# Kernel tuning notes

Hardware: AMD Instinct MI355X
Metric: run time of the kernel (lower is better)

## Reference

```python
import jax, jax.numpy as jnp
import numpy as np

B, S, H = 2, 2048, 2048
NH, NKV, HD = 16, 4, 128
GROUPS = NH // NKV
THETA = 10000.0
EPS = 1e-6


def setup_inputs() -> dict:
    key = jax.random.key(0)
    ks = jax.random.split(key, 6)
    scale = 0.02
    return {
        "hidden_states": jax.random.normal(ks[0], (B, S, H), jnp.float32),
        "wq": jax.random.normal(ks[1], (NH * HD, H), jnp.float32) * scale,
        "wk": jax.random.normal(ks[2], (NKV * HD, H), jnp.float32) * scale,
        "wv": jax.random.normal(ks[3], (NKV * HD, H), jnp.float32) * scale,
        "wo": jax.random.normal(ks[4], (H, NH * HD), jnp.float32) * scale,
        "q_norm_weight": jnp.ones((HD,), jnp.float32),
        "k_norm_weight": jnp.ones((HD,), jnp.float32),
    }


def _rope_tables(seq_len):
    inv_freq = 1.0 / (THETA ** (jnp.arange(0, HD, 2, dtype=jnp.float32) / HD))
    t = jnp.arange(seq_len, dtype=jnp.float32)
    freqs = jnp.outer(t, inv_freq)              # [S, HD/2]
    emb = jnp.concatenate([freqs, freqs], -1)   # [S, HD]
    return jnp.cos(emb), jnp.sin(emb)


def _rotate_half(x):
    x1, x2 = x[..., : HD // 2], x[..., HD // 2:]
    return jnp.concatenate([-x2, x1], -1)


def _rmsnorm(x, w):
    var = jnp.mean(jnp.square(x), axis=-1, keepdims=True)
    return x * jax.lax.rsqrt(var + EPS) * w


def reference(hidden_states, wq, wk, wv, wo, q_norm_weight, k_norm_weight):
    b, s, _ = hidden_states.shape
    q = (hidden_states @ wq.T).reshape(b, s, NH, HD).transpose(0, 2, 1, 3)    # [b,nh,s,d]
    k = (hidden_states @ wk.T).reshape(b, s, NKV, HD).transpose(0, 2, 1, 3)   # [b,nkv,s,d]
    v = (hidden_states @ wv.T).reshape(b, s, NKV, HD).transpose(0, 2, 1, 3)

    cos, sin = _rope_tables(s)                  # [s,d]
    q = q * cos + _rotate_half(q) * sin
    k = k * cos + _rotate_half(k) * sin

    # fused QK RMSNorm (applied inside fused_qknorm_flash_attention)
    q = _rmsnorm(q, q_norm_weight)
    k = _rmsnorm(k, k_norm_weight)

    # GQA: share each kv head across GROUPS query heads without materializing repeats
    qg = q.reshape(b, NKV, GROUPS, s, HD)
    scale = 1.0 / jnp.sqrt(jnp.float32(HD))
    scores = jnp.einsum('bhgqd,bhkd->bhgqk', qg, k) * scale   # [b,nkv,g,s,s]
    causal = jnp.tril(jnp.ones((s, s), bool))
    scores = jnp.where(causal, scores, jnp.finfo(scores.dtype).min)
    probs = jax.nn.softmax(scores, axis=-1)
    out = jnp.einsum('bhgqk,bhkd->bhgqd', probs, v)            # [b,nkv,g,s,d]
    out = out.reshape(b, NH, s, HD).transpose(0, 2, 1, 3).reshape(b, s, NH * HD)
    return out @ wo.T
```

## Files before the change

### kernel.cpp

```cpp
#include <hip/hip_runtime.h>
#include <math.h>

typedef __bf16 bf16;
typedef __bf16 bf16x8 __attribute__((ext_vector_type(8)));
typedef __bf16 bf16x4 __attribute__((ext_vector_type(4)));
typedef float f32x4 __attribute__((ext_vector_type(4)));

#define B_DIM 2
#define S_LEN 2048
#define H_DIM 2048
#define NH 16
#define NKV 4
#define HD 128

__device__ __forceinline__ void gl_lds16(const void* g, void* l) {
    __builtin_amdgcn_global_load_lds(
        (const __attribute__((address_space(1))) unsigned int*)g,
        (__attribute__((address_space(3))) unsigned int*)l, 16, 0, 0);
}

__global__ __launch_bounds__(256) void cast_all(const float* __restrict__ s0,
                                                const float* __restrict__ s1,
                                                const float* __restrict__ s2,
                                                const float* __restrict__ s3,
                                                const float* __restrict__ s4,
                                                bf16* __restrict__ dst) {
    const int i = blockIdx.x * 256 + threadIdx.x;
    const float* src;
    int off;
    if (i < 2097152)      { src = s0; off = 0; }
    else if (i < 3145728) { src = s1; off = 2097152; }
    else if (i < 3407872) { src = s2; off = 3145728; }
    else if (i < 3670016) { src = s3; off = 3407872; }
    else                  { src = s4; off = 3670016; }
    float4 f = ((const float4*)src)[i - off];
    bf16x4 o = { (bf16)f.x, (bf16)f.y, (bf16)f.z, (bf16)f.w };
    *(bf16x4*)(dst + (size_t)i * 4) = o;
}

template <typename OutT>
__global__ __launch_bounds__(256) void gemm_bt(const bf16* __restrict__ A,
                                               const bf16* __restrict__ Bt,
                                               OutT* __restrict__ C,
                                               int M, int N, int K) {
    __shared__ __align__(16) bf16 As[128 * 32];
    __shared__ __align__(16) bf16 Bs[128 * 32];
    const int t = threadIdx.x;
    const int lane = t & 63, w = t >> 6;
    const int wm = (w & 1) * 64, wn = (w >> 1) * 64;
    const int lr = lane & 15, quad = lane >> 4;
    const int m0 = blockIdx.x * 128, n0 = blockIdx.y * 128;
    const int lrow = lane >> 2, lk = (lane & 3) * 8;
    f32x4 acc[4][4];
#pragma unroll
    for (int i = 0; i < 4; i++)
#pragma unroll
        for (int j = 0; j < 4; j++) acc[i][j] = (f32x4){0.f, 0.f, 0.f, 0.f};

    for (int k0 = 0; k0 < K; k0 += 32) {
        __syncthreads();
#pragma unroll
        for (int i = 0; i < 2; i++) {
            const int r0 = i * 64 + w * 16;
            gl_lds16(A + (size_t)(m0 + r0 + lrow) * K + k0 + lk, &As[r0 * 32]);
            gl_lds16(Bt + (size_t)(n0 + r0 + lrow) * K + k0 + lk, &Bs[r0 * 32]);
        }
        __syncthreads();
        bf16x8 af[4], bfr[4];
#pragma unroll
        for (int i = 0; i < 4; i++) af[i] = *(const bf16x8*)&As[(wm + i * 16 + lr) * 32 + quad * 8];
#pragma unroll
        for (int j = 0; j < 4; j++) bfr[j] = *(const bf16x8*)&Bs[(wn + j * 16 + lr) * 32 + quad * 8];
#pragma unroll
        for (int i = 0; i < 4; i++)
#pragma unroll
            for (int j = 0; j < 4; j++)
                acc[i][j] = __builtin_amdgcn_mfma_f32_16x16x32_bf16(af[i], bfr[j], acc[i][j], 0, 0, 0);
    }
#pragma unroll
    for (int i = 0; i < 4; i++) {
        int m = m0 + wm + i * 16 + quad * 4;
#pragma unroll
        for (int j = 0; j < 4; j++) {
            int n = n0 + wn + j * 16 + lr;
#pragma unroll
            for (int r = 0; r < 4; r++)
                C[(size_t)(m + r) * N + n] = (OutT)acc[i][j][r];
        }
    }
}

__global__ __launch_bounds__(256) void rope_rms(const bf16* __restrict__ qkv,
                                                const float* __restrict__ qw,
                                                const float* __restrict__ kw,
                                                bf16* __restrict__ qb,
                                                bf16* __restrict__ kb,
                                                bf16* __restrict__ vt) {
    const int tok = blockIdx.x;
    const int b = tok >> 11, s = tok & (S_LEN - 1);
    const int lane = threadIdx.x & 63, w = threadIdx.x >> 6;
    const bf16* row = qkv + (size_t)tok * 3072;
    const float inv = expf(-(float)lane * (9.210340371976184f / 64.f));
    const float ang = (float)s * inv;
    float s_, c_;
    sincosf(ang, &s_, &c_);
    const float wq1 = qw[lane], wq2 = qw[lane + 64];
    const float wk1 = kw[lane], wk2 = kw[lane + 64];
    for (int u = w; u < 24; u += 4) {
        if (u < 16) {
            const float x1 = (float)row[u * 128 + lane], x2 = (float)row[u * 128 + 64 + lane];
            float y1 = x1 * c_ - x2 * s_;
            float y2 = x2 * c_ + x1 * s_;
            float ss = y1 * y1 + y2 * y2;
#pragma unroll
            for (int m = 1; m < 64; m <<= 1) ss += __shfl_xor(ss, m);
            const float r = rsqrtf(ss * (1.f / 128.f) + 1e-6f);
            size_t o = ((size_t)(b * NH + u) * S_LEN + s) * HD;
            qb[o + lane]      = (bf16)(y1 * r * wq1);
            qb[o + 64 + lane] = (bf16)(y2 * r * wq2);
        } else if (u < 20) {
            const int kh = u - 16;
            const float x1 = (float)row[2048 + kh * 128 + lane], x2 = (float)row[2048 + kh * 128 + 64 + lane];
            float y1 = x1 * c_ - x2 * s_;
            float y2 = x2 * c_ + x1 * s_;
            float ss = y1 * y1 + y2 * y2;
#pragma unroll
            for (int m = 1; m < 64; m <<= 1) ss += __shfl_xor(ss, m);
            const float r = rsqrtf(ss * (1.f / 128.f) + 1e-6f);
            size_t base = (size_t)(b * NKV + kh) * 16 * 16384;
            kb[base + (size_t)(lane >> 3) * 16384 + s * 8 + (lane & 7)]       = (bf16)(y1 * r * wk1);
            kb[base + (size_t)(8 + (lane >> 3)) * 16384 + s * 8 + (lane & 7)] = (bf16)(y2 * r * wk2);
        } else {
            const int vh = u - 20;
            const float x1 = (float)row[2560 + vh * 128 + lane], x2 = (float)row[2560 + vh * 128 + 64 + lane];
            const int m = s & 31;
            const int gi = (s >> 5) * 4 + ((m & 15) >> 2);
            const int el = ((m >> 4) << 2) | (m & 3);
            size_t base = ((size_t)(b * NKV + vh) * 256 + gi) * 1024 + el;
            vt[base + (size_t)lane * 8]        = (bf16)x1;
            vt[base + (size_t)(lane + 64) * 8] = (bf16)x2;
        }
    }
}

__global__ __launch_bounds__(256, 2) void flash(const bf16* __restrict__ qg,
                                                const bf16* __restrict__ kg,
                                                const bf16* __restrict__ vg,
                                                bf16* __restrict__ attn) {
    const int idx = blockIdx.x;
    const int g = idx >> 5;
    const int qt = (g < 8) ? (15 - g) : (g - 8);
    const int hb = idx & 31;
    const int h = hb & 15, b = hb >> 4;
    const int kvh = h >> 2;
    const bf16* qh = qg + (size_t)(b * NH + h) * S_LEN * HD;
    const bf16* kh = kg + (size_t)(b * NKV + kvh) * (16 * 16384);
    const bf16* vh = vg + (size_t)(b * NKV + kvh) * (256 * 1024);
    __shared__ __align__(16) bf16 Ks[2][16 * 512];
    __shared__ __align__(16) bf16 Vs[2][8 * 1024];
    const int t = threadIdx.x, lane = t & 63, w = t >> 6, lr = lane & 15, quad = lane >> 4;
    const int row0 = qt * 128 + w * 32;
    bf16x8 qf[2][4];
#pragma unroll
    for (int mg = 0; mg < 2; mg++)
#pragma unroll
        for (int c = 0; c < 4; c++)
            qf[mg][c] = *(const bf16x8*)(qh + (size_t)(row0 + mg * 16 + lr) * HD + c * 32 + quad * 8);
    f32x4 o[2][8];
    f32x4 lacc[2];
#pragma unroll
    for (int mg = 0; mg < 2; mg++) {
        lacc[mg] = (f32x4){0.f, 0.f, 0.f, 0.f};
#pragma unroll
        for (int j = 0; j < 8; j++) o[mg][j] = (f32x4){0.f, 0.f, 0.f, 0.f};
    }
    const bf16 one = (bf16)1.0f;
    const bf16x8 ones8 = {one, one, one, one, one, one, one, one};
    const float C1 = 0.12751744f;
    const float C2 = -17.3123405f;
    const int ntile = 2 * qt + 2;

    auto stage = [&](int kt_, int bi) {
        const int kb = kt_ * 64;
#pragma unroll
        for (int i = 0; i < 4; i++) {
            const int dc = w * 4 + i;
            gl_lds16(kh + (size_t)dc * 16384 + (size_t)kb * 8 + lane * 8, &Ks[bi][dc * 512]);
        }
#pragma unroll
        for (int i = 0; i < 2; i++) {
            const int c = w * 2 + i;
            const bf16* src = vh + (size_t)(8 * kt_ + ((c >> 2) << 2) + (c & 3)) * 1024 + lane * 8;
            gl_lds16(src, &Vs[bi][c * 1024]);
            gl_lds16(src + 512, &Vs[bi][c * 1024 + 512]);
        }
    };

    stage(0, 0);
    __syncthreads();
    int cur = 0;

    for (int kt = 0; kt < ntile; ++kt) {
        const int kbase = kt * 64;
        if (kt + 1 < ntile) stage(kt + 1, cur ^ 1);
        f32x4 sacc[2][4];
#pragma unroll
        for (int mg = 0; mg < 2; mg++)
#pragma unroll
            for (int n = 0; n < 4; n++) sacc[mg][n] = (f32x4){0.f, 0.f, 0.f, 0.f};
#pragma unroll
        for (int n = 0; n < 4; n++)
#pragma unroll
            for (int c = 0; c < 4; c++) {
                bf16x8 kf = *(const bf16x8*)&Ks[cur][(c * 4 + quad) * 512 + (n * 16 + lr) * 8];
                sacc[0][n] = __builtin_amdgcn_mfma_f32_16x16x32_bf16(kf, qf[0][c], sacc[0][n], 0, 0, 0);
                sacc[1][n] = __builtin_amdgcn_mfma_f32_16x16x32_bf16(kf, qf[1][c], sacc[1][n], 0, 0, 0);
            }
        const bool diag = (kt >= 2 * qt);
        bf16x8 pT[2][2];
#pragma unroll
        for (int mg = 0; mg < 2; mg++) {
            const int qrow = row0 + mg * 16 + lr;
#pragma unroll
            for (int n = 0; n < 4; n++)
#pragma unroll
                for (int r = 0; r < 4; r++) {
                    float ev = exp2f(fmaf(sacc[mg][n][r], C1, C2));
                    if (diag) {
                        const int key = kbase + n * 16 + quad * 4 + r;
                        ev = (key <= qrow) ? ev : 0.f;
                    }
                    pT[mg][n >> 1][(n & 1) * 4 + r] = (bf16)ev;
                }
        }
#pragma unroll
        for (int k2 = 0; k2 < 2; k2++) {
#pragma unroll
            for (int j = 0; j < 8; j++) {
                bf16x8 vf = *(const bf16x8*)&Vs[cur][(k2 * 4 + quad) * 1024 + (j * 16 + lr) * 8];
                o[0][j] = __builtin_amdgcn_mfma_f32_16x16x32_bf16(vf, pT[0][k2], o[0][j], 0, 0, 0);
                o[1][j] = __builtin_amdgcn_mfma_f32_16x16x32_bf16(vf, pT[1][k2], o[1][j], 0, 0, 0);
            }
            lacc[0] = __builtin_amdgcn_mfma_f32_16x16x32_bf16(ones8, pT[0][k2], lacc[0], 0, 0, 0);
            lacc[1] = __builtin_amdgcn_mfma_f32_16x16x32_bf16(ones8, pT[1][k2], lacc[1], 0, 0, 0);
        }
        __syncthreads();
        cur ^= 1;
    }
#pragma unroll
    for (int mg = 0; mg < 2; mg++) {
        const float inv = 1.0f / lacc[mg][0];
        const int qrow = row0 + mg * 16 + lr;
        bf16* dst = attn + ((size_t)(b * S_LEN) + qrow) * (NH * HD) + h * HD + quad * 4;
#pragma unroll
        for (int j = 0; j < 8; j++) {
            bf16x4 st = { (bf16)(o[mg][j][0] * inv), (bf16)(o[mg][j][1] * inv),
                          (bf16)(o[mg][j][2] * inv), (bf16)(o[mg][j][3] * inv) };
            *(bf16x4*)(dst + j * 16) = st;
        }
    }
}

extern "C" void kernel_launch(void* const* d_in, const int* in_sizes, int n_in,
                              void* d_out, int out_size, void* d_ws, size_t ws_size,
                              hipStream_t stream) {
    (void)in_sizes; (void)n_in; (void)out_size; (void)ws_size;
    const float* hs  = (const float*)d_in[0];
    const float* wq  = (const float*)d_in[1];
    const float* wk  = (const float*)d_in[2];
    const float* wv  = (const float*)d_in[3];
    const float* wo  = (const float*)d_in[4];
    const float* qnw = (const float*)d_in[5];
    const float* knw = (const float*)d_in[6];
    float* out = (float*)d_out;

    char* ws = (char*)d_ws;
    size_t off = 0;
    auto alloc = [&](size_t bytes) {
        void* p = ws + off;
        off += (bytes + 255) & ~(size_t)255;
        return p;
    };
    bf16* hs_bf   = (bf16*)alloc((size_t)4096 * 2048 * 2);
    bf16* wqkv_bf = (bf16*)alloc((size_t)3072 * 2048 * 2);
    bf16* wo_bf   = (bf16*)alloc((size_t)2048 * 2048 * 2);
    bf16* qkv_bf  = (bf16*)alloc((size_t)4096 * 3072 * 2);
    bf16* q_bf    = (bf16*)alloc((size_t)B_DIM * NH * S_LEN * HD * 2);
    bf16* k_bf    = (bf16*)alloc((size_t)B_DIM * NKV * S_LEN * HD * 2);
    bf16* vt_bf   = (bf16*)alloc((size_t)B_DIM * NKV * S_LEN * HD * 2);
    bf16* at_bf   = (bf16*)alloc((size_t)4096 * 2048 * 2);

    cast_all<<<18432, 256, 0, stream>>>(hs, wq, wk, wv, wo, hs_bf);
    gemm_bt<bf16><<<dim3(32, 24), 256, 0, stream>>>(hs_bf, wqkv_bf, qkv_bf, 4096, 3072, 2048);
    rope_rms<<<4096, 256, 0, stream>>>(qkv_bf, qnw, knw, q_bf, k_bf, vt_bf);
    flash<<<dim3(512), 256, 0, stream>>>(q_bf, k_bf, vt_bf, at_bf);
    gemm_bt<float><<<dim3(32, 16), 256, 0, stream>>>(at_bf, wo_bf, out, 4096, 2048, 2048);
}
```

Measured before the change: 325.3 us.

## Replace 128x128 GEMM with 256x256 double-buffered 8-wave pipelined GEMM

Replaces the simple 128x128-tile, single-buffered GEMM with a 256x256-tile kernel using 512 threads, 128 KB of LDS, and double-buffered global-to-LDS loads interleaved with MFMA phases. It also adds an XOR swizzle on LDS columns to avoid bank conflicts, a workgroup remapping across XCDs, and s_setprio around the MFMA bursts. The aim is more data reuse per tile and overlap of loads with compute. In exchange the grid is small (192 and 128 blocks), which may underfill the 256 CUs, and the hand-rolled waitcnt and barrier scheme is fragile.

```diff
diff --git a/kernel.cpp b/kernel.cpp
--- a/kernel.cpp
+++ b/kernel.cpp
@@ -17,6 +17,12 @@
     __builtin_amdgcn_global_load_lds(
         (const __attribute__((address_space(1))) unsigned int*)g,
         (__attribute__((address_space(3))) unsigned int*)l, 16, 0, 0);
+}
+
+__device__ __forceinline__ void bar() {
+    asm volatile("" ::: "memory");
+    __builtin_amdgcn_s_barrier();
+    asm volatile("" ::: "memory");
 }
 
 __global__ __launch_bounds__(256) void cast_all(const float* __restrict__ s0,
@@ -39,53 +45,135 @@
 }
 
 template <typename OutT>
-__global__ __launch_bounds__(256) void gemm_bt(const bf16* __restrict__ A,
-                                               const bf16* __restrict__ Bt,
-                                               OutT* __restrict__ C,
-                                               int M, int N, int K) {
-    __shared__ __align__(16) bf16 As[128 * 32];
-    __shared__ __align__(16) bf16 Bs[128 * 32];
-    const int t = threadIdx.x;
-    const int lane = t & 63, w = t >> 6;
-    const int wm = (w & 1) * 64, wn = (w >> 1) * 64;
+__global__ __launch_bounds__(512, 2) void gemm256(const bf16* __restrict__ A,
+                                                  const bf16* __restrict__ Bt,
+                                                  OutT* __restrict__ C,
+                                                  int M, int N, int K) {
+    __shared__ __align__(16) bf16 smem[65536];
+    const int t = threadIdx.x, lane = t & 63, w = t >> 6;
     const int lr = lane & 15, quad = lane >> 4;
-    const int m0 = blockIdx.x * 128, n0 = blockIdx.y * 128;
-    const int lrow = lane >> 2, lk = (lane & 3) * 8;
-    f32x4 acc[4][4];
-#pragma unroll
-    for (int i = 0; i < 4; i++)
+    const int nN = N >> 8;
+    const int nwg = gridDim.x, chunk = nwg >> 3;
+    const int bid = blockIdx.x;
+    const int lid = (bid & 7) * chunk + (bid >> 3);
+    const int m0 = (lid / nN) << 8, n0 = (lid % nN) << 8;
+    const int mh_w = w >> 2;
+    const int wn = (w & 3) << 6;
+    const int nh_w = (w & 3) >> 1;
+    const int rb = (w & 1) << 6;
+    const int nK = K >> 6;
+    const int nIter = K >> 7;
+
+    const int ld0 = w * 2;
+    const int lrow = lane >> 2;
+    const int csrc = (lane & 3) ^ ((lane >> 5) << 1);
+    const int swz = (lr >> 3) << 1;
+
+    auto stA = [&](int ts, int mh) {
+        if (ts < nK) {
+            bf16* db = smem + (ts & 1) * 16384 + mh * 8192;
+            const bf16* sp = A + (size_t)(m0 + mh * 128) * K + ts * 64;
+#pragma unroll
+            for (int i = 0; i < 2; i++) {
+                const int ldi = ld0 + i, kb = ldi >> 3, rg = ldi & 7;
+                gl_lds16(sp + (size_t)(rg * 16 + lrow) * K + kb * 32 + csrc * 8,
+                         db + kb * 4096 + rg * 512);
+            }
+        }
+    };
+    auto stB = [&](int ts, int nh) {
+        if (ts < nK) {
+            bf16* db = smem + 32768 + (ts & 1) * 16384 + nh * 8192;
+            const bf16* sp = Bt + (size_t)(n0 + nh * 128) * K + ts * 64;
+#pragma unroll
+            for (int i = 0; i < 2; i++) {
+                const int ldi = ld0 + i, kb = ldi >> 3, rg = ldi & 7;
+                gl_lds16(sp + (size_t)(rg * 16 + lrow) * K + kb * 32 + csrc * 8,
+                         db + kb * 4096 + rg * 512);
+            }
+        }
+    };
+
+    f32x4 acc[8][4];
+#pragma unroll
+    for (int i = 0; i < 8; i++)
 #pragma unroll
         for (int j = 0; j < 4; j++) acc[i][j] = (f32x4){0.f, 0.f, 0.f, 0.f};
-
-    for (int k0 = 0; k0 < K; k0 += 32) {
-        __syncthreads();
-#pragma unroll
-        for (int i = 0; i < 2; i++) {
-            const int r0 = i * 64 + w * 16;
-            gl_lds16(A + (size_t)(m0 + r0 + lrow) * K + k0 + lk, &As[r0 * 32]);
-            gl_lds16(Bt + (size_t)(n0 + r0 + lrow) * K + k0 + lk, &Bs[r0 * 32]);
-        }
-        __syncthreads();
-        bf16x8 af[4], bfr[4];
-#pragma unroll
-        for (int i = 0; i < 4; i++) af[i] = *(const bf16x8*)&As[(wm + i * 16 + lr) * 32 + quad * 8];
-#pragma unroll
-        for (int j = 0; j < 4; j++) bfr[j] = *(const bf16x8*)&Bs[(wn + j * 16 + lr) * 32 + quad * 8];
-#pragma unroll
-        for (int i = 0; i < 4; i++)
-#pragma unroll
-            for (int j = 0; j < 4; j++)
-                acc[i][j] = __builtin_amdgcn_mfma_f32_16x16x32_bf16(af[i], bfr[j], acc[i][j], 0, 0, 0);
-    }
-#pragma unroll
-    for (int i = 0; i < 4; i++) {
-        int m = m0 + wm + i * 16 + quad * 4;
-#pragma unroll
-        for (int j = 0; j < 4; j++) {
-            int n = n0 + wn + j * 16 + lr;
+    bf16x8 af[8], b0[4], b1[4];
+
+    auto rdA = [&](int s, int fi0) {
+        const bf16* bp = smem + s * 16384 + mh_w * 8192;
+#pragma unroll
+        for (int f = 0; f < 4; f++)
+#pragma unroll
+            for (int ks = 0; ks < 2; ks++)
+                af[f * 2 + ks] = *(const bf16x8*)(bp + ks * 4096 +
+                                                  ((fi0 + f) * 16 + lr) * 32 + (quad ^ swz) * 8);
+    };
+    auto rdB = [&](int s, int fj0, bf16x8* dst) {
+        const bf16* bp = smem + 32768 + s * 16384 + nh_w * 8192;
+#pragma unroll
+        for (int f = 0; f < 2; f++)
+#pragma unroll
+            for (int ks = 0; ks < 2; ks++)
+                dst[f * 2 + ks] = *(const bf16x8*)(bp + ks * 4096 +
+                                                   (rb + (fj0 + f) * 16 + lr) * 32 + (quad ^ swz) * 8);
+    };
+    auto mm16 = [&](int fi0, int fj0, bf16x8* bb) {
+        __builtin_amdgcn_s_setprio(1);
+#pragma unroll
+        for (int f = 0; f < 4; f++)
+#pragma unroll
+            for (int g = 0; g < 2; g++)
+#pragma unroll
+                for (int ks = 0; ks < 2; ks++)
+                    acc[fi0 + f][fj0 + g] = __builtin_amdgcn_mfma_f32_16x16x32_bf16(
+                        af[f * 2 + ks], bb[g * 2 + ks], acc[fi0 + f][fj0 + g], 0, 0, 0);
+        __builtin_amdgcn_s_setprio(0);
+    };
+
+    stA(0, 0); stA(0, 1); stB(0, 0); stB(0, 1); stA(1, 0);
+    asm volatile("s_waitcnt vmcnt(2)" ::: "memory");
+    bar();
+
+    for (int i = 0; i < nIter; i++) {
+        const int ts0 = 2 * i;
+#pragma unroll
+        for (int h = 0; h < 2; h++) {
+            const int ts = ts0 + h, s = h;
+            rdA(s, 0); rdB(s, 0, b0);
+            stA(ts + 1, 1);
+            bar();
+            mm16(0, 0, b0);
+            bar();
+            rdB(s, 2, b1);
+            stB(ts + 1, 0);
+            bar();
+            mm16(0, 2, b1);
+            bar();
+            rdA(s, 4);
+            stB(ts + 1, 1);
+            bar();
+            mm16(4, 2, b1);
+            bar();
+            rdB(s, 0, b0);
+            stA(ts + 2, 0);
+            bar();
+            mm16(4, 0, b0);
+            if (ts + 2 < nK) asm volatile("s_waitcnt vmcnt(2)" ::: "memory");
+            else             asm volatile("s_waitcnt vmcnt(0)" ::: "memory");
+            bar();
+        }
+    }
+#pragma unroll
+    for (int fi = 0; fi < 8; fi++) {
+        const int m = m0 + mh_w * 128 + fi * 16 + quad * 4;
+#pragma unroll
+        for (int fj = 0; fj < 4; fj++) {
+            const int n = n0 + wn + fj * 16 + lr;
 #pragma unroll
             for (int r = 0; r < 4; r++)
-                C[(size_t)(m + r) * N + n] = (OutT)acc[i][j][r];
+                C[(size_t)(m + r) * N + n] = (OutT)acc[fi][fj][r];
         }
     }
 }
@@ -291,8 +379,8 @@
     bf16* at_bf   = (bf16*)alloc((size_t)4096 * 2048 * 2);
 
     cast_all<<<18432, 256, 0, stream>>>(hs, wq, wk, wv, wo, hs_bf);
-    gemm_bt<bf16><<<dim3(32, 24), 256, 0, stream>>>(hs_bf, wqkv_bf, qkv_bf, 4096, 3072, 2048);
+    gemm256<bf16><<<dim3(192), 512, 0, stream>>>(hs_bf, wqkv_bf, qkv_bf, 4096, 3072, 2048);
     rope_rms<<<4096, 256, 0, stream>>>(qkv_bf, qnw, knw, q_bf, k_bf, vt_bf);
     flash<<<dim3(512), 256, 0, stream>>>(q_bf, k_bf, vt_bf, at_bf);
-    gemm_bt<float><<<dim3(32, 16), 256, 0, stream>>>(at_bf, wo_bf, out, 4096, 2048, 2048);
-}
+    gemm256<float><<<dim3(128), 512, 0, stream>>>(at_bf, wo_bf, out, 4096, 2048, 2048);
+}
```

Result: no change. 321.5 us (-1.2%).
